# Performance work log

Measured on AMD Instinct MI355X. Metric: run time of the kernel, lower is better.

## Reference

```python
import jax, jax.numpy as jnp
import numpy as np

N = 100000   # nodes
E = 1000000  # edges
IN = 100     # input feature dim
H = 4        # heads
D = 32       # hidden per head (H*D = 128)
C = 47       # classes
EPS = 1e-5
SLOPE = 0.2  # DGL GATv2 leaky_relu negative slope


def setup_inputs() -> dict:
    key = jax.random.key(0)
    ks = jax.random.split(key, 32)
    lin = lambda k, i, o: (jax.random.normal(k, (i, o), jnp.float32) / np.float32(np.sqrt(i)))
    inp = {}
    inp['x'] = jax.random.normal(ks[0], (N, IN), jnp.float32)
    inp['src'] = jax.random.randint(ks[1], (E,), 0, N, jnp.int32)
    inp['dst'] = jnp.sort(jax.random.randint(ks[2], (E,), 0, N, jnp.int32))
    # layer 0: IN -> H*D, Linear residual (IN != H*D)
    inp['Wsrc0'] = lin(ks[3], IN, H * D); inp['bsrc0'] = jnp.zeros(H * D, jnp.float32)
    inp['Wdst0'] = lin(ks[4], IN, H * D); inp['bdst0'] = jnp.zeros(H * D, jnp.float32)
    inp['attn0'] = lin(ks[5], H, D)
    inp['Wres0'] = lin(ks[6], IN, H * D); inp['bres0'] = jnp.zeros(H * D, jnp.float32)
    # layer 1: H*D -> H*D, Identity residual (128 == 128)
    inp['Wsrc1'] = lin(ks[7], H * D, H * D); inp['bsrc1'] = jnp.zeros(H * D, jnp.float32)
    inp['Wdst1'] = lin(ks[8], H * D, H * D); inp['bdst1'] = jnp.zeros(H * D, jnp.float32)
    inp['attn1'] = lin(ks[9], H, D)
    # layer 2: H*D -> H*C, Linear residual (128 != 188)
    inp['Wsrc2'] = lin(ks[10], H * D, H * C); inp['bsrc2'] = jnp.zeros(H * C, jnp.float32)
    inp['Wdst2'] = lin(ks[11], H * D, H * C); inp['bdst2'] = jnp.zeros(H * C, jnp.float32)
    inp['attn2'] = lin(ks[12], H, C)
    inp['Wres2'] = lin(ks[13], H * D, H * C); inp['bres2'] = jnp.zeros(H * C, jnp.float32)
    # BatchNorm1d params (training-mode batch stats)
    inp['g0'] = jnp.ones(H * D, jnp.float32); inp['be0'] = jnp.zeros(H * D, jnp.float32)
    inp['g1'] = jnp.ones(H * D, jnp.float32); inp['be1'] = jnp.zeros(H * D, jnp.float32)
    return inp


def _gatv2(h, src, dst, Ws, bs, Wd, bd, attn, resval):
    """One GATv2Conv on a full block (src feats == dst feats == h)."""
    Hh, Dd = attn.shape
    fs = (h @ Ws + bs).reshape(-1, Hh, Dd)   # [N,H,D] src projection
    fd = (h @ Wd + bd).reshape(-1, Hh, Dd)   # [N,H,D] dst projection
    e = jax.nn.leaky_relu(fs[src] + fd[dst], SLOPE)         # [E,H,D]
    logits = jnp.einsum('ehd,hd->eh', e, attn)              # [E,H]
    m = jax.ops.segment_max(logits, dst, num_segments=N)    # per-dst max
    ex = jnp.exp(logits - m[dst])
    s = jax.ops.segment_sum(ex, dst, num_segments=N)
    alpha = ex / s[dst]                                      # edge softmax
    out = jax.ops.segment_sum(alpha[:, :, None] * fs[src], dst, num_segments=N)
    return out + resval                                      # [N,H,D]


def _bn(x, g, b):
    mu = x.mean(0)
    v = x.var(0)  # biased, as torch BN training mode
    return g * (x - mu) / jnp.sqrt(v + EPS) + b


def reference(x, src, dst,
              Wsrc0, bsrc0, Wdst0, bdst0, attn0, Wres0, bres0,
              Wsrc1, bsrc1, Wdst1, bdst1, attn1,
              Wsrc2, bsrc2, Wdst2, bdst2, attn2, Wres2, bres2,
              g0, be0, g1, be1):
    # layer 0: conv(+relu activation) -> flatten -> BN -> relu (dropout = eval identity)
    res0 = (x @ Wres0 + bres0).reshape(N, H, D)
    h = jax.nn.relu(_gatv2(x, src, dst, Wsrc0, bsrc0, Wdst0, bdst0, attn0, res0))
    h = jax.nn.relu(_bn(h.reshape(N, H * D), g0, be0))
    # layer 1: Identity residual
    res1 = h.reshape(N, H, D)
    h = jax.nn.relu(_gatv2(h, src, dst, Wsrc1, bsrc1, Wdst1, bdst1, attn1, res1))
    h = jax.nn.relu(_bn(h.reshape(N, H * D), g1, be1))
    # layer 2: no activation; mean over heads; log_softmax
    res2 = (h @ Wres2 + bres2).reshape(N, H, C)
    h = _gatv2(h, src, dst, Wsrc2, bsrc2, Wdst2, bdst2, attn2, res2)
    h = h.mean(1)                                # [N,C]
    return jax.nn.log_softmax(h, axis=-1)
```

## Files before the change

### kernel.cpp

```cpp
#include <hip/hip_runtime.h>
#include <hip/hip_bf16.h>

#define Nn 100000
#define Ee 1000000
#define INF_ 100
#define Hh 4
#define Dd 32
#define HD 128
#define Cc 47
#define HC 188
#define HCP 192
#define EPSV 1e-5f
#define SLOPE 0.2f

typedef __hip_bfloat16 bf16;
typedef __attribute__((ext_vector_type(8))) short short8;
typedef __attribute__((ext_vector_type(4))) float f32x4;

__device__ __forceinline__ float tof(bf16 v) { return __bfloat162float(v); }
__device__ __forceinline__ float b2f(unsigned short u) {
    return __uint_as_float((unsigned)u << 16);
}
__device__ __forceinline__ float ldb(const bf16* p) {
    return b2f(*(const unsigned short*)p);
}
__device__ __forceinline__ unsigned short f2u(float v) {
    bf16 t = __float2bfloat16(v);
    return *(unsigned short*)&t;
}

__global__ void detect_dtype(const unsigned* __restrict__ x, int* __restrict__ flag) {
    if (blockIdx.x == 0 && threadIdx.x == 0) {
        int good = 0;
        for (int i = 0; i < 256; ++i) {
            unsigned lo = x[i] & 0xFFFFu;
            float v = __uint_as_float(lo << 16);
            float a = fabsf(v);
            if (a > 1e-4f && a < 10.f) good++;
        }
        *flag = (good >= 128) ? 1 : 0;
    }
}

__device__ __forceinline__ float ld_any(const void* p, int i, int isbf) {
    return isbf ? tof(((const bf16*)p)[i]) : ((const float*)p)[i];
}

__global__ void cvt_x(const void* __restrict__ in, bf16* __restrict__ out,
                      const int* __restrict__ flag) {
    int i = blockIdx.x * blockDim.x + threadIdx.x;
    if (i >= Nn * 128) return;
    int row = i >> 7, col = i & 127;
    float v = (col < INF_) ? ld_any(in, row * INF_ + col, *flag) : 0.f;
    out[i] = __float2bfloat16(v);
}

#define NSP 15
struct CvtTab { const void* src[NSP]; int off[NSP + 1]; };

__global__ void cvt_params(CvtTab t, bf16* __restrict__ out, int total,
                           const int* __restrict__ flag) {
    int i = blockIdx.x * blockDim.x + threadIdx.x;
    if (i >= total) return;
    int isbf = *flag;
    int seg = 0;
    while (i >= t.off[seg + 1]) seg++;
    out[i] = __float2bfloat16(ld_any(t.src[seg], i - t.off[seg], isbf));
}

#define WROWS 1280
struct PrepTab { const void* src[8]; int row0[8]; int K[8]; int M[8]; int MP[8]; };

__global__ void prep_all(PrepTab t, bf16* __restrict__ wtb, const int* __restrict__ flag) {
    int i = blockIdx.x * blockDim.x + threadIdx.x;
    if (i >= WROWS * 128) return;
    int row = i >> 7, k = i & 127;
    int isbf = *flag;
    float v = 0.f;
#pragma unroll
    for (int q = 0; q < 8; ++q) {
        if (row >= t.row0[q] && row < t.row0[q] + t.MP[q]) {
            int m = row - t.row0[q];
            if (m < t.M[q] && k < t.K[q])
                v = ld_any(t.src[q], k * t.M[q] + m, isbf);
        }
    }
    wtb[i] = __float2bfloat16(v);
}

__global__ void zero_u32(unsigned* __restrict__ p, int n) {
    int i = blockIdx.x * blockDim.x + threadIdx.x;
    if (i < n) p[i] = 0u;
}

__global__ void build_ptr(const int* __restrict__ dst, int* __restrict__ ptr) {
    int n = blockIdx.x * blockDim.x + threadIdx.x;
    if (n > Nn) return;
    if (n == Nn) { ptr[Nn] = Ee; return; }
    int lo = 0, hi = Ee;
    while (lo < hi) {
        int mid = (lo + hi) >> 1;
        if (dst[mid] < n) lo = mid + 1; else hi = mid;
    }
    ptr[n] = lo;
}

template <int MP, int NOUT, int CS, bool ABN, bool PAD47, int OSTR>
__global__ __launch_bounds__(256, 4) void gemm_big(
    const bf16* __restrict__ A, const bf16* __restrict__ Wt,
    const bf16* __restrict__ b0, const bf16* __restrict__ b1,
    const bf16* __restrict__ b2,
    bf16* __restrict__ o0, bf16* __restrict__ o1, bf16* __restrict__ o2,
    int MR, const float* __restrict__ bnp) {
    __shared__ __align__(16) bf16 Al[64 * 136];
    const int row0 = blockIdx.x * 64;
    const int tid = threadIdx.x;
#pragma unroll
    for (int j = 0; j < 4; ++j) {
        int idx = tid + j * 256;
        int r = idx >> 4, kk = (idx & 15) * 8;
        int4 val = {0, 0, 0, 0};
        if (row0 + r < Nn) {
            val = *(const int4*)&A[(size_t)(row0 + r) * 128 + kk];
            if (ABN) {
                short8 av = *(short8*)&val;
                bf16 tmp[8];
#pragma unroll
                for (int u = 0; u < 8; ++u) {
                    float v = b2f((unsigned short)av[u]);
                    v = fmaxf(fmaf(v, bnp[kk + u], bnp[128 + kk + u]), 0.f);
                    tmp[u] = __float2bfloat16(v);
                }
                val = *(int4*)tmp;
            }
        }
        *(int4*)&Al[r * 136 + kk] = val;
    }
    __syncthreads();
    const int wave = tid >> 6, lane = tid & 63;
    const int n16 = lane & 15, quad = lane >> 4;
    const int colbase = blockIdx.y * (64 * CS) + wave * (16 * CS);
    f32x4 acc[4][CS];
#pragma unroll
    for (int rt = 0; rt < 4; ++rt)
#pragma unroll
        for (int c = 0; c < CS; ++c) acc[rt][c] = (f32x4){0.f, 0.f, 0.f, 0.f};
    const bf16* wb[CS];
#pragma unroll
    for (int c = 0; c < CS; ++c)
        wb[c] = Wt + (size_t)(colbase + c * 16 + n16) * 128 + quad * 8;
    const bf16* ap = Al + n16 * 136 + quad * 8;
#pragma unroll
    for (int ks = 0; ks < 4; ++ks) {
        short8 bf[CS];
#pragma unroll
        for (int c = 0; c < CS; ++c) bf[c] = *(const short8*)(wb[c] + ks * 32);
#pragma unroll
        for (int rt = 0; rt < 4; ++rt) {
            short8 af = *(const short8*)(ap + rt * 16 * 136 + ks * 32);
#pragma unroll
            for (int c = 0; c < CS; ++c)
                acc[rt][c] = __builtin_amdgcn_mfma_f32_16x16x32_bf16(af, bf[c], acc[rt][c], 0, 0, 0);
        }
    }
#pragma unroll
    for (int c = 0; c < CS; ++c) {
        int col = colbase + c * 16 + n16;
        int oi = col / MP, lc = col - oi * MP;
        if (oi >= NOUT || lc >= MR) continue;
        const bf16* bp = (oi == 0) ? b0 : (oi == 1) ? b1 : b2;
        bf16* o = (oi == 0) ? o0 : (oi == 1) ? o1 : o2;
        float bb = tof(bp[lc]);
        int st = PAD47 ? (lc + lc / 47) : lc;
#pragma unroll
        for (int rt = 0; rt < 4; ++rt) {
#pragma unroll
            for (int i = 0; i < 4; ++i) {
                int row = row0 + rt * 16 + quad * 4 + i;
                if (row < Nn)
                    o[(size_t)row * OSTR + st] = __float2bfloat16(acc[rt][c][i] + bb);
            }
        }
    }
}

template <bool RESBN>
__global__ __launch_bounds__(256) void gat_fused_128(
    const bf16* __restrict__ fs, const bf16* __restrict__ fd,
    const int* __restrict__ srcI, const int* __restrict__ ptr,
    const bf16* __restrict__ attn, const bf16* __restrict__ resb,
    const float* __restrict__ bnp, bf16* __restrict__ hout) {
    const int wave = threadIdx.x >> 6, lane = threadIdx.x & 63;
    const int d = blockIdx.x * 4 + wave;
    if (d >= Nn) return;
    const int c0 = lane * 2;
    ushort2 aq = *(const ushort2*)&attn[c0];
    float a0 = b2f(aq.x), a1 = b2f(aq.y);
    ushort2 dq = *(const ushort2*)&fd[(size_t)d * HD + c0];
    float fd0 = b2f(dq.x), fd1 = b2f(dq.y);
    float l = 0.f, O0 = 0.f, O1 = 0.f;
    int e = ptr[d];
    const int e1 = ptr[d + 1];
    for (; e + 3 < e1; e += 4) {
        int sA = srcI[e], sB = srcI[e + 1], sC = srcI[e + 2], sD = srcI[e + 3];
        ushort2 qA = *(const ushort2*)&fs[(size_t)sA * HD + c0];
        ushort2 qB = *(const ushort2*)&fs[(size_t)sB * HD + c0];
        ushort2 qC = *(const ushort2*)&fs[(size_t)sC * HD + c0];
        ushort2 qD = *(const ushort2*)&fs[(size_t)sD * HD + c0];
        float fA0 = b2f(qA.x), fA1 = b2f(qA.y);
        float fB0 = b2f(qB.x), fB1 = b2f(qB.y);
        float fC0 = b2f(qC.x), fC1 = b2f(qC.y);
        float fD0 = b2f(qD.x), fD1 = b2f(qD.y);
        float tA0 = fA0 + fd0; tA0 = fmaxf(tA0, tA0 * SLOPE);
        float tA1 = fA1 + fd1; tA1 = fmaxf(tA1, tA1 * SLOPE);
        float tB0 = fB0 + fd0; tB0 = fmaxf(tB0, tB0 * SLOPE);
        float tB1 = fB1 + fd1; tB1 = fmaxf(tB1, tB1 * SLOPE);
        float tC0 = fC0 + fd0; tC0 = fmaxf(tC0, tC0 * SLOPE);
        float tC1 = fC1 + fd1; tC1 = fmaxf(tC1, tC1 * SLOPE);
        float tD0 = fD0 + fd0; tD0 = fmaxf(tD0, tD0 * SLOPE);
        float tD1 = fD1 + fd1; tD1 = fmaxf(tD1, tD1 * SLOPE);
        float pA = fmaf(tA0, a0, tA1 * a1);
        float pB = fmaf(tB0, a0, tB1 * a1);
        float pC = fmaf(tC0, a0, tC1 * a1);
        float pD = fmaf(tD0, a0, tD1 * a1);
        pA += __shfl_xor(pA, 1); pB += __shfl_xor(pB, 1);
        pC += __shfl_xor(pC, 1); pD += __shfl_xor(pD, 1);
        pA += __shfl_xor(pA, 2); pB += __shfl_xor(pB, 2);
        pC += __shfl_xor(pC, 2); pD += __shfl_xor(pD, 2);
        pA += __shfl_xor(pA, 4); pB += __shfl_xor(pB, 4);
        pC += __shfl_xor(pC, 4); pD += __shfl_xor(pD, 4);
        pA += __shfl_xor(pA, 8); pB += __shfl_xor(pB, 8);
        pC += __shfl_xor(pC, 8); pD += __shfl_xor(pD, 8);
        float eA = __expf(pA), eB = __expf(pB), eC = __expf(pC), eD = __expf(pD);
        l += (eA + eB) + (eC + eD);
        O0 = fmaf(eA, fA0, O0); O0 = fmaf(eB, fB0, O0);
        O0 = fmaf(eC, fC0, O0); O0 = fmaf(eD, fD0, O0);
        O1 = fmaf(eA, fA1, O1); O1 = fmaf(eB, fB1, O1);
        O1 = fmaf(eC, fC1, O1); O1 = fmaf(eD, fD1, O1);
    }
    for (; e < e1; ++e) {
        int s = srcI[e];
        ushort2 fq = *(const ushort2*)&fs[(size_t)s * HD + c0];
        float f0 = b2f(fq.x), f1 = b2f(fq.y);
        float t0 = f0 + fd0; t0 = fmaxf(t0, t0 * SLOPE);
        float t1 = f1 + fd1; t1 = fmaxf(t1, t1 * SLOPE);
        float p = fmaf(t0, a0, t1 * a1);
        p += __shfl_xor(p, 1); p += __shfl_xor(p, 2);
        p += __shfl_xor(p, 4); p += __shfl_xor(p, 8);
        float pe = __expf(p);
        l += pe;
        O0 = fmaf(pe, f0, O0);
        O1 = fmaf(pe, f1, O1);
    }
    float inv = l > 0.f ? 1.f / l : 0.f;
    ushort2 rq = *(const ushort2*)&resb[(size_t)d * HD + c0];
    float r0 = b2f(rq.x), r1 = b2f(rq.y);
    if (RESBN) {
        r0 = fmaxf(fmaf(r0, bnp[c0], bnp[HD + c0]), 0.f);
        r1 = fmaxf(fmaf(r1, bnp[c0 + 1], bnp[HD + c0 + 1]), 0.f);
    }
    float v0 = fmaxf(fmaf(O0, inv, r0), 0.f);
    float v1 = fmaxf(fmaf(O1, inv, r1), 0.f);
    ushort2 ov; ov.x = f2u(v0); ov.y = f2u(v1);
    *(ushort2*)&hout[(size_t)d * HD + c0] = ov;
}

__global__ __launch_bounds__(256) void gat_fused_188(
    const bf16* __restrict__ fs, const bf16* __restrict__ fd,
    const int* __restrict__ srcI, const int* __restrict__ ptr,
    const bf16* __restrict__ attn, const bf16* __restrict__ rs,
    void* __restrict__ out, const int* __restrict__ flag) {
    const int wave = threadIdx.x >> 6, lane = threadIdx.x & 63;
    const int d = blockIdx.x * 4 + wave;
    if (d >= Nn) return;
    const int h = lane >> 4, j = lane & 15;
    const int c0 = h * 48 + j;
    const int ca = h * Cc + j;
    const bool has2 = (j < 15);
    float a0 = ldb(&attn[ca]);
    float a1 = ldb(&attn[ca + 16]);
    float a2 = has2 ? ldb(&attn[ca + 32]) : 0.f;
    const bf16* fdr = fd + (size_t)d * HCP;
    float fd0 = ldb(&fdr[c0]);
    float fd1 = ldb(&fdr[c0 + 16]);
    float fd2 = ldb(&fdr[c0 + 32]);
    float l = 0.f, O0 = 0.f, O1 = 0.f, O2 = 0.f;
    int e = ptr[d];
    const int e1 = ptr[d + 1];
    for (; e + 1 < e1; e += 2) {
        int sa = srcI[e], sb = srcI[e + 1];
        const bf16* fra = fs + (size_t)sa * HCP;
        const bf16* frb = fs + (size_t)sb * HCP;
        float fa0 = ldb(&fra[c0]), fb0 = ldb(&frb[c0]);
        float fa1 = ldb(&fra[c0 + 16]), fb1 = ldb(&frb[c0 + 16]);
        float fa2 = ldb(&fra[c0 + 32]), fb2 = ldb(&frb[c0 + 32]);
        float ta0 = fa0 + fd0; ta0 = fmaxf(ta0, ta0 * SLOPE);
        float ta1 = fa1 + fd1; ta1 = fmaxf(ta1, ta1 * SLOPE);
        float ta2 = fa2 + fd2; ta2 = fmaxf(ta2, ta2 * SLOPE);
        float tb0 = fb0 + fd0; tb0 = fmaxf(tb0, tb0 * SLOPE);
        float tb1 = fb1 + fd1; tb1 = fmaxf(tb1, tb1 * SLOPE);
        float tb2 = fb2 + fd2; tb2 = fmaxf(tb2, tb2 * SLOPE);
        float pa = fmaf(ta0, a0, fmaf(ta1, a1, ta2 * a2));
        float pb = fmaf(tb0, a0, fmaf(tb1, a1, tb2 * a2));
        pa += __shfl_xor(pa, 1); pb += __shfl_xor(pb, 1);
        pa += __shfl_xor(pa, 2); pb += __shfl_xor(pb, 2);
        pa += __shfl_xor(pa, 4); pb += __shfl_xor(pb, 4);
        pa += __shfl_xor(pa, 8); pb += __shfl_xor(pb, 8);
        float ea = __expf(pa), eb = __expf(pb);
        l += ea + eb;
        O0 = fmaf(ea, fa0, O0); O0 = fmaf(eb, fb0, O0);
        O1 = fmaf(ea, fa1, O1); O1 = fmaf(eb, fb1, O1);
        O2 = fmaf(ea, fa2, O2); O2 = fmaf(eb, fb2, O2);
    }
    if (e < e1) {
        int s = srcI[e];
        const bf16* fr = fs + (size_t)s * HCP;
        float f0 = ldb(&fr[c0]);
        float f1 = ldb(&fr[c0 + 16]);
        float f2 = ldb(&fr[c0 + 32]);
        float t0 = f0 + fd0; t0 = fmaxf(t0, t0 * SLOPE);
        float t1 = f1 + fd1; t1 = fmaxf(t1, t1 * SLOPE);
        float t2 = f2 + fd2; t2 = fmaxf(t2, t2 * SLOPE);
        float p = fmaf(t0, a0, fmaf(t1, a1, t2 * a2));
        p += __shfl_xor(p, 1); p += __shfl_xor(p, 2);
        p += __shfl_xor(p, 4); p += __shfl_xor(p, 8);
        float pe = __expf(p);
        l += pe;
        O0 = fmaf(pe, f0, O0);
        O1 = fmaf(pe, f1, O1);
        O2 = fmaf(pe, f2, O2);
    }
    float inv = l > 0.f ? 1.f / l : 0.f;
    const bf16* rr = rs + (size_t)d * HCP;
    float v0 = fmaf(O0, inv, ldb(&rr[c0]));
    float v1 = fmaf(O1, inv, ldb(&rr[c0 + 16]));
    float v2 = has2 ? fmaf(O2, inv, ldb(&rr[c0 + 32])) : 0.f;
    v0 += __shfl_xor(v0, 16); v0 += __shfl_xor(v0, 32); v0 *= 0.25f;
    v1 += __shfl_xor(v1, 16); v1 += __shfl_xor(v1, 32); v1 *= 0.25f;
    v2 += __shfl_xor(v2, 16); v2 += __shfl_xor(v2, 32); v2 *= 0.25f;
    float mx = fmaxf(v0, v1);
    if (has2) mx = fmaxf(mx, v2);
    mx = fmaxf(mx, __shfl_xor(mx, 1)); mx = fmaxf(mx, __shfl_xor(mx, 2));
    mx = fmaxf(mx, __shfl_xor(mx, 4)); mx = fmaxf(mx, __shfl_xor(mx, 8));
    float sm = __expf(v0 - mx) + __expf(v1 - mx) + (has2 ? __expf(v2 - mx) : 0.f);
    sm += __shfl_xor(sm, 1); sm += __shfl_xor(sm, 2);
    sm += __shfl_xor(sm, 4); sm += __shfl_xor(sm, 8);
    if (h == 0) {
        float ls = mx + logf(sm);
        if (*flag) {
            bf16* o = (bf16*)out + (size_t)d * Cc;
            o[j] = __float2bfloat16(v0 - ls);
            o[j + 16] = __float2bfloat16(v1 - ls);
            if (has2) o[j + 32] = __float2bfloat16(v2 - ls);
        } else {
            float* o = (float*)out + (size_t)d * Cc;
            o[j] = v0 - ls;
            o[j + 16] = v1 - ls;
            if (has2) o[j + 32] = v2 - ls;
        }
    }
}

__global__ void col_stats(const bf16* __restrict__ in, float* __restrict__ sums) {
    int c = threadIdx.x;
    int r0 = blockIdx.x * 256;
    int r1 = r0 + 256; if (r1 > Nn) r1 = Nn;
    float s = 0.f, s2 = 0.f;
    for (int r = r0; r < r1; ++r) {
        float v = ldb(&in[(size_t)r * HD + c]);
        s += v; s2 += v * v;
    }
    atomicAdd(&sums[c], s);
    atomicAdd(&sums[HD + c], s2);
}

__global__ void bn_finalize(const float* __restrict__ sums, const bf16* __restrict__ g,
                            const bf16* __restrict__ be, float* __restrict__ ss) {
    int c = threadIdx.x;
    float mu = sums[c] * (1.f / Nn);
    float var = sums[HD + c] * (1.f / Nn) - mu * mu;
    float sc = tof(g[c]) * rsqrtf(var + EPSV);
    ss[c] = sc;
    ss[HD + c] = tof(be[c]) - mu * sc;
}

extern "C" void kernel_launch(void* const* d_in, const int* in_sizes, int n_in,
                              void* d_out, int out_size, void* d_ws, size_t ws_size,
                              hipStream_t stream) {
    (void)in_sizes; (void)n_in; (void)out_size; (void)ws_size;
    const void* x = d_in[0];
    const int* src = (const int*)d_in[1];
    const int* dst = (const int*)d_in[2];

    char* ws = (char*)d_ws;
    size_t off = 0;
    auto alloc = [&](size_t bytes) {
        void* p = ws + off;
        off += (bytes + 255) & ~(size_t)255;
        return p;
    };
    bf16* xb = (bf16*)alloc((size_t)Nn * 128 * 2);
    bf16* rb = (bf16*)alloc((size_t)Nn * HD * 2);
    bf16* rs = xb;
    bf16* fs = (bf16*)alloc((size_t)Nn * HCP * 2);
    bf16* fd = (bf16*)alloc((size_t)Nn * HCP * 2);
    bf16* hbA = (bf16*)alloc((size_t)Nn * HD * 2);
    bf16* hbB = (bf16*)alloc((size_t)Nn * HD * 2);
    int* ptr = (int*)alloc((Nn + 1) * 4);
    bf16* wtb = (bf16*)alloc((size_t)WROWS * 128 * 2);
    float* bns = (float*)alloc(2 * HD * 4);
    float* bnss0 = (float*)alloc(2 * HD * 4);
    float* bnss1 = (float*)alloc(2 * HD * 4);
    bf16* pb = (bf16*)alloc(4096 * 2);
    int* flag = (int*)alloc(256);

    static const int spIdx[NSP] = {4, 6, 7, 9, 11, 13, 14, 16, 18, 19, 21, 22, 23, 24, 25};
    static const int spSz[NSP]  = {HD, HD, HD, HD, HD, HD, HD, HC, HC, HC, HC, HD, HD, HD, HD};
    CvtTab tab;
    int tot = 0;
    for (int i = 0; i < NSP; ++i) { tab.src[i] = d_in[spIdx[i]]; tab.off[i] = tot; tot += spSz[i]; }
    tab.off[NSP] = tot;
    const bf16 *bsrc0 = pb + tab.off[0], *bdst0 = pb + tab.off[1], *attn0 = pb + tab.off[2],
               *bres0 = pb + tab.off[3], *bsrc1 = pb + tab.off[4], *bdst1 = pb + tab.off[5],
               *attn1 = pb + tab.off[6], *bsrc2 = pb + tab.off[7], *bdst2 = pb + tab.off[8],
               *attn2 = pb + tab.off[9], *bres2 = pb + tab.off[10],
               *g0 = pb + tab.off[11], *be0 = pb + tab.off[12],
               *g1 = pb + tab.off[13], *be1 = pb + tab.off[14];

    PrepTab pt;
    static const int wIdx[8] = {3, 5, 8, 10, 12, 15, 17, 20};
    static const int wK[8]   = {INF_, INF_, INF_, HD, HD, HD, HD, HD};
    static const int wM[8]   = {HD, HD, HD, HD, HD, HC, HC, HC};
    static const int wMP[8]  = {128, 128, 128, 128, 128, 192, 192, 192};
    static const int wR0[8]  = {0, 128, 256, 384, 512, 640, 832, 1024};
    for (int i = 0; i < 8; ++i) {
        pt.src[i] = d_in[wIdx[i]]; pt.row0[i] = wR0[i];
        pt.K[i] = wK[i]; pt.M[i] = wM[i]; pt.MP[i] = wMP[i];
    }

    detect_dtype<<<1, 64, 0, stream>>>((const unsigned*)x, flag);
    cvt_x<<<(Nn * 128 + 255) / 256, 256, 0, stream>>>(x, xb, flag);
    cvt_params<<<(tot + 255) / 256, 256, 0, stream>>>(tab, pb, tot, flag);
    prep_all<<<(WROWS * 128 + 255) / 256, 256, 0, stream>>>(pt, wtb, flag);
    build_ptr<<<(Nn + 256) / 256, 256, 0, stream>>>(dst, ptr);

    const int fusedGrid = (Nn + 3) / 4;
    const int statsGrid = (Nn + 255) / 256;
    const int rowBlk = (Nn + 63) / 64;

    gemm_big<128, 3, 3, false, false, HD><<<dim3(rowBlk, 2), 256, 0, stream>>>(
        xb, wtb, bsrc0, bdst0, bres0, fs, fd, rb, HD, nullptr);
    gat_fused_128<false><<<fusedGrid, 256, 0, stream>>>(fs, fd, src, ptr, attn0,
                                                        rb, nullptr, hbA);
    zero_u32<<<1, 256, 0, stream>>>((unsigned*)bns, 2 * HD);
    col_stats<<<statsGrid, 128, 0, stream>>>(hbA, bns);
    bn_finalize<<<1, HD, 0, stream>>>(bns, g0, be0, bnss0);

    gemm_big<128, 2, 2, true, false, HD><<<dim3(rowBlk, 2), 256, 0, stream>>>(
        hbA, wtb + (size_t)384 * 128, bsrc1, bdst1, nullptr, fs, fd, nullptr, HD, bnss0);
    gat_fused_128<true><<<fusedGrid, 256, 0, stream>>>(fs, fd, src, ptr, attn1,
                                                       hbA, bnss0, hbB);
    zero_u32<<<1, 256, 0, stream>>>((unsigned*)bns, 2 * HD);
    col_stats<<<statsGrid, 128, 0, stream>>>(hbB, bns);
    bn_finalize<<<1, HD, 0, stream>>>(bns, g1, be1, bnss1);

    gemm_big<192, 3, 3, true, true, HCP><<<dim3(rowBlk, 3), 256, 0, stream>>>(
        hbB, wtb + (size_t)640 * 128, bsrc2, bdst2, bres2, fs, fd, rs, HC, bnss1);
    gat_fused_188<<<fusedGrid, 256, 0, stream>>>(fs, fd, src, ptr, attn2, rs,
                                                 d_out, flag);
}
```

Baseline: 698.2 us.

## Repack layer-2 features into 4-slot groups for vectorized per-lane gathers

The layer-2 projections are now stored with a 256-element row stride. Each head's 47 channels are packed as groups of three inside four-element slots, so every lane fetches its three channels with a single 8-byte load instead of three scattered 2-byte loads. The GEMM epilogue writes this layout, a small kernel repacks the attention vector the same way, and the output scatter is adjusted to match. The aim is fewer load instructions per gathered edge, at the cost of about a third more bytes per gathered row. Buffers are re-aliased (hbB shares rb, rs spills past xb into hbA) to fit the larger stride.

```diff
diff --git a/kernel.cpp b/kernel.cpp
--- a/kernel.cpp
+++ b/kernel.cpp
@@ -9,7 +9,7 @@
 #define HD 128
 #define Cc 47
 #define HC 188
-#define HCP 192
+#define HCS 256
 #define EPSV 1e-5f
 #define SLOPE 0.2f
 
@@ -66,6 +66,14 @@
     int seg = 0;
     while (i >= t.off[seg + 1]) seg++;
     out[i] = __float2bfloat16(ld_any(t.src[seg], i - t.off[seg], isbf));
+}
+
+__global__ void pack_attn(const bf16* __restrict__ a2, bf16* __restrict__ out) {
+    int i = threadIdx.x;
+    int h = i >> 6, r = i & 63, j = r >> 2, t = r & 3;
+    int cc = 3 * j + t;
+    float v = (t < 3 && cc < Cc) ? tof(a2[h * Cc + cc]) : 0.f;
+    out[i] = __float2bfloat16(v);
 }
 
 #define WROWS 1280
@@ -171,7 +179,11 @@
         const bf16* bp = (oi == 0) ? b0 : (oi == 1) ? b1 : b2;
         bf16* o = (oi == 0) ? o0 : (oi == 1) ? o1 : o2;
         float bb = tof(bp[lc]);
-        int st = PAD47 ? (lc + lc / 47) : lc;
+        int st = lc;
+        if (PAD47) {
+            int head = lc / 47, cc = lc - head * 47;
+            st = head * 64 + (cc / 3) * 4 + (cc - (cc / 3) * 3);
+        }
 #pragma unroll
         for (int rt = 0; rt < 4; ++rt) {
 #pragma unroll
@@ -268,32 +280,27 @@
 __global__ __launch_bounds__(256) void gat_fused_188(
     const bf16* __restrict__ fs, const bf16* __restrict__ fd,
     const int* __restrict__ srcI, const int* __restrict__ ptr,
-    const bf16* __restrict__ attn, const bf16* __restrict__ rs,
+    const bf16* __restrict__ attnP, const bf16* __restrict__ rs,
     void* __restrict__ out, const int* __restrict__ flag) {
     const int wave = threadIdx.x >> 6, lane = threadIdx.x & 63;
     const int d = blockIdx.x * 4 + wave;
     if (d >= Nn) return;
     const int h = lane >> 4, j = lane & 15;
-    const int c0 = h * 48 + j;
-    const int ca = h * Cc + j;
+    const int sl = lane * 4;
     const bool has2 = (j < 15);
-    float a0 = ldb(&attn[ca]);
-    float a1 = ldb(&attn[ca + 16]);
-    float a2 = has2 ? ldb(&attn[ca + 32]) : 0.f;
-    const bf16* fdr = fd + (size_t)d * HCP;
-    float fd0 = ldb(&fdr[c0]);
-    float fd1 = ldb(&fdr[c0 + 16]);
-    float fd2 = ldb(&fdr[c0 + 32]);
+    ushort4 aq = *(const ushort4*)&attnP[sl];
+    float a0 = b2f(aq.x), a1 = b2f(aq.y), a2 = b2f(aq.z);
+    ushort4 dq = *(const ushort4*)&fd[(size_t)d * HCS + sl];
+    float fd0 = b2f(dq.x), fd1 = b2f(dq.y), fd2 = b2f(dq.z);
     float l = 0.f, O0 = 0.f, O1 = 0.f, O2 = 0.f;
     int e = ptr[d];
     const int e1 = ptr[d + 1];
     for (; e + 1 < e1; e += 2) {
         int sa = srcI[e], sb = srcI[e + 1];
-        const bf16* fra = fs + (size_t)sa * HCP;
-        const bf16* frb = fs + (size_t)sb * HCP;
-        float fa0 = ldb(&fra[c0]), fb0 = ldb(&frb[c0]);
-        float fa1 = ldb(&fra[c0 + 16]), fb1 = ldb(&frb[c0 + 16]);
-        float fa2 = ldb(&fra[c0 + 32]), fb2 = ldb(&frb[c0 + 32]);
+        ushort4 qa = *(const ushort4*)&fs[(size_t)sa * HCS + sl];
+        ushort4 qb = *(const ushort4*)&fs[(size_t)sb * HCS + sl];
+        float fa0 = b2f(qa.x), fa1 = b2f(qa.y), fa2 = b2f(qa.z);
+        float fb0 = b2f(qb.x), fb1 = b2f(qb.y), fb2 = b2f(qb.z);
         float ta0 = fa0 + fd0; ta0 = fmaxf(ta0, ta0 * SLOPE);
         float ta1 = fa1 + fd1; ta1 = fmaxf(ta1, ta1 * SLOPE);
         float ta2 = fa2 + fd2; ta2 = fmaxf(ta2, ta2 * SLOPE);
@@ -314,10 +321,8 @@
     }
     if (e < e1) {
         int s = srcI[e];
-        const bf16* fr = fs + (size_t)s * HCP;
-        float f0 = ldb(&fr[c0]);
-        float f1 = ldb(&fr[c0 + 16]);
-        float f2 = ldb(&fr[c0 + 32]);
+        ushort4 fq = *(const ushort4*)&fs[(size_t)s * HCS + sl];
+        float f0 = b2f(fq.x), f1 = b2f(fq.y), f2 = b2f(fq.z);
         float t0 = f0 + fd0; t0 = fmaxf(t0, t0 * SLOPE);
         float t1 = f1 + fd1; t1 = fmaxf(t1, t1 * SLOPE);
         float t2 = f2 + fd2; t2 = fmaxf(t2, t2 * SLOPE);
@@ -331,10 +336,10 @@
         O2 = fmaf(pe, f2, O2);
     }
     float inv = l > 0.f ? 1.f / l : 0.f;
-    const bf16* rr = rs + (size_t)d * HCP;
-    float v0 = fmaf(O0, inv, ldb(&rr[c0]));
-    float v1 = fmaf(O1, inv, ldb(&rr[c0 + 16]));
-    float v2 = has2 ? fmaf(O2, inv, ldb(&rr[c0 + 32])) : 0.f;
+    ushort4 rq = *(const ushort4*)&rs[(size_t)d * HCS + sl];
+    float v0 = fmaf(O0, inv, b2f(rq.x));
+    float v1 = fmaf(O1, inv, b2f(rq.y));
+    float v2 = has2 ? fmaf(O2, inv, b2f(rq.z)) : 0.f;
     v0 += __shfl_xor(v0, 16); v0 += __shfl_xor(v0, 32); v0 *= 0.25f;
     v1 += __shfl_xor(v1, 16); v1 += __shfl_xor(v1, 32); v1 *= 0.25f;
     v2 += __shfl_xor(v2, 16); v2 += __shfl_xor(v2, 32); v2 *= 0.25f;
@@ -347,16 +352,17 @@
     sm += __shfl_xor(sm, 4); sm += __shfl_xor(sm, 8);
     if (h == 0) {
         float ls = mx + logf(sm);
+        int c = 3 * j;
         if (*flag) {
             bf16* o = (bf16*)out + (size_t)d * Cc;
-            o[j] = __float2bfloat16(v0 - ls);
-            o[j + 16] = __float2bfloat16(v1 - ls);
-            if (has2) o[j + 32] = __float2bfloat16(v2 - ls);
+            o[c] = __float2bfloat16(v0 - ls);
+            o[c + 1] = __float2bfloat16(v1 - ls);
+            if (has2) o[c + 2] = __float2bfloat16(v2 - ls);
         } else {
             float* o = (float*)out + (size_t)d * Cc;
-            o[j] = v0 - ls;
-            o[j + 16] = v1 - ls;
-            if (has2) o[j + 32] = v2 - ls;
+            o[c] = v0 - ls;
+            o[c + 1] = v1 - ls;
+            if (has2) o[c + 2] = v2 - ls;
         }
     }
 }
@@ -400,18 +406,19 @@
         return p;
     };
     bf16* xb = (bf16*)alloc((size_t)Nn * 128 * 2);
+    bf16* hbA = (bf16*)alloc((size_t)Nn * HD * 2);
     bf16* rb = (bf16*)alloc((size_t)Nn * HD * 2);
+    bf16* hbB = rb;
     bf16* rs = xb;
-    bf16* fs = (bf16*)alloc((size_t)Nn * HCP * 2);
-    bf16* fd = (bf16*)alloc((size_t)Nn * HCP * 2);
-    bf16* hbA = (bf16*)alloc((size_t)Nn * HD * 2);
-    bf16* hbB = (bf16*)alloc((size_t)Nn * HD * 2);
+    bf16* fs = (bf16*)alloc((size_t)Nn * HCS * 2);
+    bf16* fd = (bf16*)alloc((size_t)Nn * HCS * 2);
     int* ptr = (int*)alloc((Nn + 1) * 4);
     bf16* wtb = (bf16*)alloc((size_t)WROWS * 128 * 2);
     float* bns = (float*)alloc(2 * HD * 4);
     float* bnss0 = (float*)alloc(2 * HD * 4);
     float* bnss1 = (float*)alloc(2 * HD * 4);
     bf16* pb = (bf16*)alloc(4096 * 2);
+    bf16* attn2p = (bf16*)alloc(256 * 2);
     int* flag = (int*)alloc(256);
 
     static const int spIdx[NSP] = {4, 6, 7, 9, 11, 13, 14, 16, 18, 19, 21, 22, 23, 24, 25};
@@ -441,6 +448,7 @@
     detect_dtype<<<1, 64, 0, stream>>>((const unsigned*)x, flag);
     cvt_x<<<(Nn * 128 + 255) / 256, 256, 0, stream>>>(x, xb, flag);
     cvt_params<<<(tot + 255) / 256, 256, 0, stream>>>(tab, pb, tot, flag);
+    pack_attn<<<1, 256, 0, stream>>>(attn2, attn2p);
     prep_all<<<(WROWS * 128 + 255) / 256, 256, 0, stream>>>(pt, wtb, flag);
     build_ptr<<<(Nn + 256) / 256, 256, 0, stream>>>(dst, ptr);
 
@@ -464,8 +472,8 @@
     col_stats<<<statsGrid, 128, 0, stream>>>(hbB, bns);
     bn_finalize<<<1, HD, 0, stream>>>(bns, g1, be1, bnss1);
 
-    gemm_big<192, 3, 3, true, true, HCP><<<dim3(rowBlk, 3), 256, 0, stream>>>(
+    gemm_big<192, 3, 3, true, true, HCS><<<dim3(rowBlk, 3), 256, 0, stream>>>(
         hbB, wtb + (size_t)640 * 128, bsrc2, bdst2, bres2, fs, fd, rs, HC, bnss1);
-    gat_fused_188<<<fusedGrid, 256, 0, stream>>>(fs, fd, src, ptr, attn2, rs,
+    gat_fused_188<<<fusedGrid, 256, 0, stream>>>(fs, fd, src, ptr, attn2p, rs,
                                                  d_out, flag);
 }
```

New measurement: 707.6 us. About the same (+1.4%).
